# Performance work log

Hardware: AMD Instinct MI355X
Metric: run time of the kernel (lower is better)

## Reference

```python
import jax, jax.numpy as jnp
import numpy as np

N_NODES = 200000
N_PATCHES = 256
TIMESTEPS = 12
NHID = 16
HORIZON = 12
IN_DIM = NHID * TIMESTEPS + TIMESTEPS  # 204


def setup_inputs() -> dict:
    key = jax.random.key(0)
    ks = jax.random.split(key, 6)
    mixer_x = jax.random.normal(ks[0], (1, TIMESTEPS, N_PATCHES, NHID), dtype=jnp.float32)
    features = jax.random.normal(ks[1], (N_NODES, TIMESTEPS), dtype=jnp.float32)
    W1 = jax.random.normal(ks[2], (IN_DIM, IN_DIM), dtype=jnp.float32) * (1.0 / np.sqrt(IN_DIM))
    b1 = jnp.zeros((IN_DIM,), dtype=jnp.float32)
    W2 = jax.random.normal(ks[3], (IN_DIM, HORIZON), dtype=jnp.float32) * (1.0 / np.sqrt(IN_DIM))
    b2 = jnp.zeros((HORIZON,), dtype=jnp.float32)
    node_patch = jax.random.randint(ks[4], (N_NODES,), 0, N_PATCHES, dtype=jnp.int32)
    return {"mixer_x": mixer_x, "features": features, "W1": W1, "b1": b1,
            "W2": W2, "b2": b2, "node_patch": node_patch}


def reference(mixer_x, features, W1, b1, W2, b2, node_patch):
    # mixer_x: (b, t, p, f) -> per-patch flattened features 'b p (t f)'
    b, t, p, f = mixer_x.shape
    patch_feat = jnp.transpose(mixer_x, (0, 2, 1, 3)).reshape(b, p, t * f)
    # per-node gather of its patch's features: (b, N, t*f)
    g = jnp.take(patch_feat, node_patch, axis=1)
    # node features broadcast over batch: (b, N, t)
    node_x = jnp.broadcast_to(features[None], (b,) + features.shape)
    x = jnp.concatenate([g, node_x], axis=-1)  # (b, N, in_dim)
    h = jax.nn.relu(jnp.einsum('bni,ij->bnj', x, W1) + b1)
    out = jnp.einsum('bnh,ho->bno', h, W2) + b2  # (1, N, horizon)
    return out
```

## Files before the change

kernel.cpp:

```cpp
#include <hip/hip_runtime.h>
#include <hip/hip_bf16.h>

#define N_NODES   200000
#define N_PATCHES 256
#define TSTEPS    12
#define NHID      16
#define HORIZON   12
#define GDIM      192
#define IN_DIM    204
#define NCHUNKS   6250
#define K2_THREADS 512
#define TOTAL_WAVES 2048
#define TBL_U4    6528

typedef __attribute__((ext_vector_type(8)))  short        bf16x8;
typedef __attribute__((ext_vector_type(16))) float        f32x16;
typedef __attribute__((ext_vector_type(4)))  unsigned int u32x4;

__device__ __forceinline__ unsigned int pk2(float lo, float hi) {
    unsigned short l = __builtin_bit_cast(unsigned short, __float2bfloat16(lo));
    unsigned short h = __builtin_bit_cast(unsigned short, __float2bfloat16(hi));
    return ((unsigned int)h << 16) | (unsigned int)l;
}

__device__ __forceinline__ bf16x8 frag_of(unsigned int a, unsigned int b,
                                          unsigned int c, unsigned int d) {
    u32x4 u; u[0] = a; u[1] = b; u[2] = c; u[3] = d;
    return __builtin_bit_cast(bf16x8, u);
}

__device__ __forceinline__ float bf16bits_lo(unsigned int w) {
    return __builtin_bit_cast(float, w << 16);
}
__device__ __forceinline__ float bf16bits_hi(unsigned int w) {
    return __builtin_bit_cast(float, w & 0xffff0000u);
}

__device__ __forceinline__ void gload_lds16(const uint4* g, uint4* l) {
    __builtin_amdgcn_global_load_lds(
        (const __attribute__((address_space(1))) unsigned int*)g,
        (__attribute__((address_space(3))) unsigned int*)l,
        16, 0, 0);
}

__device__ __forceinline__ float ldW1f(const float* __restrict__ W1, int k, int j) {
    const bool ok = (k < TSTEPS) && (j < IN_DIM);
    const int  idx = ok ? ((GDIM + k) * IN_DIM + j) : 0;
    const float v = W1[idx];
    return ok ? v : 0.0f;
}
__device__ __forceinline__ float ldW2t(const float* __restrict__ W2, int j, int o) {
    const bool ok = (j < IN_DIM) && (o < HORIZON);
    const int  idx = ok ? (j * HORIZON + o) : 0;
    const float v = W2[idx];
    return ok ? v : 0.0f;
}

__global__ __launch_bounds__(1024) void precompute(
    const float* __restrict__ mixer_x,
    const float* __restrict__ W1,
    const float* __restrict__ b1,
    const float* __restrict__ W2,
    unsigned short* __restrict__ patch_hb,
    u32x4* __restrict__ wfrag)
{
    const int blk = blockIdx.x;
    const int tid = threadIdx.x;

    if (blk == N_PATCHES) {
        const int lane = tid & 63;
        const int g    = tid >> 6;
        const int jl   = lane & 31;
        const int kb   = 4 * (lane >> 5);
        for (int f = g; f < 20; f += 16) {
            u32x4 u;
            if (f < 7) {
                const int j = f * 32 + jl;
                u[0] = pk2(ldW1f(W1, kb + 0,  j), ldW1f(W1, kb + 1,  j));
                u[1] = pk2(ldW1f(W1, kb + 2,  j), ldW1f(W1, kb + 3,  j));
                u[2] = pk2(ldW1f(W1, kb + 8,  j), ldW1f(W1, kb + 9,  j));
                u[3] = pk2(ldW1f(W1, kb + 10, j), ldW1f(W1, kb + 11, j));
            } else {
                const int j0 = (f - 7) * 16 + kb;
                u[0] = pk2(ldW2t(W2, j0 + 0,  jl), ldW2t(W2, j0 + 1,  jl));
                u[1] = pk2(ldW2t(W2, j0 + 2,  jl), ldW2t(W2, j0 + 3,  jl));
                u[2] = pk2(ldW2t(W2, j0 + 8,  jl), ldW2t(W2, j0 + 9,  jl));
                u[3] = pk2(ldW2t(W2, j0 + 10, jl), ldW2t(W2, j0 + 11, jl));
            }
            wfrag[f * 64 + lane] = u;
        }
        return;
    }

    __shared__ float xs[GDIM];
    __shared__ float partial[3 * IN_DIM];
    const int p = blk;
    const int j = tid & 255;
    const int q = tid >> 8;

    if (tid < GDIM) {
        const int t = tid >> 4, f = tid & 15;
        xs[tid] = mixer_x[(t * N_PATCHES + p) * NHID + f];
    }
    __syncthreads();

    float acc = 0.0f;
    if (j < IN_DIM) {
        acc = (q == 0) ? b1[j] : 0.0f;
        const int ibase = q * 48;
#pragma unroll 16
        for (int i = 0; i < 48; ++i)
            acc = fmaf(xs[ibase + i], W1[(ibase + i) * IN_DIM + j], acc);
        if (q > 0) partial[(q - 1) * IN_DIM + j] = acc;
    }
    __syncthreads();
    if (q == 0 && j < IN_DIM) {
        const float v = acc + partial[j] + partial[IN_DIM + j] + partial[2 * IN_DIM + j];
        patch_hb[p * IN_DIM + j] =
            __builtin_bit_cast(unsigned short, __float2bfloat16(v));
    }
}

__global__ __launch_bounds__(512) void node_mlp_mfma(
    const float* __restrict__ features,
    const int*   __restrict__ node_patch,
    const unsigned short* __restrict__ patch_hb,
    const u32x4* __restrict__ wfrag,
    const float* __restrict__ b2,
    float* __restrict__ out)
{
    __shared__ unsigned short smem[N_PATCHES * IN_DIM];

    const int tid  = threadIdx.x;
    const int lane = tid & 63;
    const int wid  = tid >> 6;
    const int jl   = lane & 31;
    const int hi   = lane >> 5;

    int c = blockIdx.x * 8 + wid;
    float4 fa, fb, fc; int p;
    {
        const float4* fp = (const float4*)(features + (c * 32 + jl) * TSTEPS);
        fa = fp[0]; fb = fp[1]; fc = fp[2];
        p  = node_patch[c * 32 + jl];
    }

    bf16x8 A1f[7], A2f[13];
#pragma unroll
    for (int f = 0; f < 7; ++f)
        A1f[f] = __builtin_bit_cast(bf16x8, wfrag[f * 64 + lane]);
#pragma unroll
    for (int f = 0; f < 13; ++f)
        A2f[f] = __builtin_bit_cast(bf16x8, wfrag[(7 + f) * 64 + lane]);

    const float4 b2A = *(const float4*)(b2 + 4 * hi);
    const float4 b2B = *(const float4*)(b2 + 8);

    {
        const uint4* src = (const uint4*)patch_hb;
        uint4* dst = (uint4*)smem;
#pragma unroll
        for (int k = 0; k < 13; ++k) {
            const int i = tid + k * K2_THREADS;
            if (i < TBL_U4) gload_lds16(src + i, dst + i);
        }
    }
    __syncthreads();

    while (true) {
        const int  cn    = c + TOTAL_WAVES;
        const bool haveN = (cn < NCHUNKS);
        float4 fa2, fb2, fc2; int p2 = 0;
        if (haveN) {
            const float4* fq = (const float4*)(features + (cn * 32 + jl) * TSTEPS);
            fa2 = fq[0]; fb2 = fq[1]; fc2 = fq[2];
            p2  = node_patch[cn * 32 + jl];
        }

        const bf16x8 B1 = frag_of(hi ? pk2(fb.x, fb.y) : pk2(fa.x, fa.y),
                                  hi ? pk2(fb.z, fb.w) : pk2(fa.z, fa.w),
                                  hi ? 0u              : pk2(fc.x, fc.y),
                                  hi ? 0u              : pk2(fc.z, fc.w));

        const unsigned short* row = smem + p * IN_DIM;

        f32x16 oE, oO;
#pragma unroll
        for (int e = 0; e < 16; ++e) { oE[e] = 0.0f; oO[e] = 0.0f; }

#pragma unroll
        for (int t = 0; t < 7; ++t) {
            f32x16 acc;
#pragma unroll
            for (int G = 0; G < 4; ++G) {
                const int eoff = t * 32 + 8 * G + 4 * hi;
                const bool ok  = (eoff <= 200);
                const uint2 r  = *(const uint2*)(row + (ok ? eoff : 0));
                acc[4 * G + 0] = ok ? bf16bits_lo(r.x) : 0.0f;
                acc[4 * G + 1] = ok ? bf16bits_hi(r.x) : 0.0f;
                acc[4 * G + 2] = ok ? bf16bits_lo(r.y) : 0.0f;
                acc[4 * G + 3] = ok ? bf16bits_hi(r.y) : 0.0f;
            }

            acc = __builtin_amdgcn_mfma_f32_32x32x16_bf16(A1f[t], B1, acc, 0, 0, 0);

            const bf16x8 ba = frag_of(
                pk2(fmaxf(acc[0], 0.f), fmaxf(acc[1], 0.f)),
                pk2(fmaxf(acc[2], 0.f), fmaxf(acc[3], 0.f)),
                pk2(fmaxf(acc[4], 0.f), fmaxf(acc[5], 0.f)),
                pk2(fmaxf(acc[6], 0.f), fmaxf(acc[7], 0.f)));
            oE = __builtin_amdgcn_mfma_f32_32x32x16_bf16(A2f[2 * t], ba, oE, 0, 0, 0);

            if (t < 6) {
                const bf16x8 bb = frag_of(
                    pk2(fmaxf(acc[8],  0.f), fmaxf(acc[9],  0.f)),
                    pk2(fmaxf(acc[10], 0.f), fmaxf(acc[11], 0.f)),
                    pk2(fmaxf(acc[12], 0.f), fmaxf(acc[13], 0.f)),
                    pk2(fmaxf(acc[14], 0.f), fmaxf(acc[15], 0.f)));
                oO = __builtin_amdgcn_mfma_f32_32x32x16_bf16(A2f[2 * t + 1], bb, oO, 0, 0, 0);
            }
        }

        {
            const int node = c * 32 + jl;
            float* orow = out + node * HORIZON;
            const float s0 = oE[0] + oO[0], s1 = oE[1] + oO[1];
            const float s2 = oE[2] + oO[2], s3 = oE[3] + oO[3];
            if (hi == 0) {
                const float s4 = oE[4] + oO[4], s5 = oE[5] + oO[5];
                const float s6 = oE[6] + oO[6], s7 = oE[7] + oO[7];
                *(float4*)(orow + 0) = make_float4(s0 + b2A.x, s1 + b2A.y,
                                                   s2 + b2A.z, s3 + b2A.w);
                *(float4*)(orow + 8) = make_float4(s4 + b2B.x, s5 + b2B.y,
                                                   s6 + b2B.z, s7 + b2B.w);
            } else {
                *(float4*)(orow + 4) = make_float4(s0 + b2A.x, s1 + b2A.y,
                                                   s2 + b2A.z, s3 + b2A.w);
            }
        }

        if (!haveN) break;
        fa = fa2; fb = fb2; fc = fc2; p = p2; c = cn;
    }
}

extern "C" void kernel_launch(void* const* d_in, const int* in_sizes, int n_in,
                              void* d_out, int out_size, void* d_ws, size_t ws_size,
                              hipStream_t stream) {
    const float* mixer_x    = (const float*)d_in[0];
    const float* features   = (const float*)d_in[1];
    const float* W1         = (const float*)d_in[2];
    const float* b1         = (const float*)d_in[3];
    const float* W2         = (const float*)d_in[4];
    const float* b2         = (const float*)d_in[5];
    const int*   node_patch = (const int*)d_in[6];
    float* out = (float*)d_out;

    unsigned short* patch_hb = (unsigned short*)d_ws;
    u32x4*          wfrag    = (u32x4*)((char*)d_ws + 104448);

    precompute<<<257, 1024, 0, stream>>>(mixer_x, W1, b1, W2, patch_hb, wfrag);

    node_mlp_mfma<<<256, K2_THREADS, 0, stream>>>(features, node_patch,
                                                  patch_hb, wfrag, b2, out);
}
```

Before: 25.84 us.

## Use 768-thread blocks, hardware bf16 pack instruction, and single output accumulator

```diff
diff --git a/kernel.cpp b/kernel.cpp
--- a/kernel.cpp
+++ b/kernel.cpp
@@ -9,8 +9,8 @@
 #define GDIM      192
 #define IN_DIM    204
 #define NCHUNKS   6250
-#define K2_THREADS 512
-#define TOTAL_WAVES 2048
+#define K2_THREADS 768
+#define K2_WAVES_TOTAL 3072
 #define TBL_U4    6528
 
 typedef __attribute__((ext_vector_type(8)))  short        bf16x8;
@@ -21,6 +21,12 @@
     unsigned short l = __builtin_bit_cast(unsigned short, __float2bfloat16(lo));
     unsigned short h = __builtin_bit_cast(unsigned short, __float2bfloat16(hi));
     return ((unsigned int)h << 16) | (unsigned int)l;
+}
+
+__device__ __forceinline__ unsigned int cvtpk(float lo, float hi) {
+    unsigned int r;
+    asm("v_cvt_pk_bf16_f32 %0, %1, %2" : "=v"(r) : "v"(lo), "v"(hi));
+    return r;
 }
 
 __device__ __forceinline__ bf16x8 frag_of(unsigned int a, unsigned int b,
@@ -121,7 +127,7 @@
     }
 }
 
-__global__ __launch_bounds__(512) void node_mlp_mfma(
+__global__ __launch_bounds__(K2_THREADS) void node_mlp_mfma(
     const float* __restrict__ features,
     const int*   __restrict__ node_patch,
     const unsigned short* __restrict__ patch_hb,
@@ -137,7 +143,7 @@
     const int jl   = lane & 31;
     const int hi   = lane >> 5;
 
-    int c = blockIdx.x * 8 + wid;
+    int c = blockIdx.x * 12 + wid;
     float4 fa, fb, fc; int p;
     {
         const float4* fp = (const float4*)(features + (c * 32 + jl) * TSTEPS);
@@ -160,7 +166,7 @@
         const uint4* src = (const uint4*)patch_hb;
         uint4* dst = (uint4*)smem;
 #pragma unroll
-        for (int k = 0; k < 13; ++k) {
+        for (int k = 0; k < 9; ++k) {
             const int i = tid + k * K2_THREADS;
             if (i < TBL_U4) gload_lds16(src + i, dst + i);
         }
@@ -168,7 +174,7 @@
     __syncthreads();
 
     while (true) {
-        const int  cn    = c + TOTAL_WAVES;
+        const int  cn    = c + K2_WAVES_TOTAL;
         const bool haveN = (cn < NCHUNKS);
         float4 fa2, fb2, fc2; int p2 = 0;
         if (haveN) {
@@ -177,16 +183,16 @@
             p2  = node_patch[cn * 32 + jl];
         }
 
-        const bf16x8 B1 = frag_of(hi ? pk2(fb.x, fb.y) : pk2(fa.x, fa.y),
-                                  hi ? pk2(fb.z, fb.w) : pk2(fa.z, fa.w),
-                                  hi ? 0u              : pk2(fc.x, fc.y),
-                                  hi ? 0u              : pk2(fc.z, fc.w));
+        const bf16x8 B1 = frag_of(hi ? cvtpk(fb.x, fb.y) : cvtpk(fa.x, fa.y),
+                                  hi ? cvtpk(fb.z, fb.w) : cvtpk(fa.z, fa.w),
+                                  hi ? 0u                : cvtpk(fc.x, fc.y),
+                                  hi ? 0u                : cvtpk(fc.z, fc.w));
 
         const unsigned short* row = smem + p * IN_DIM;
 
-        f32x16 oE, oO;
-#pragma unroll
-        for (int e = 0; e < 16; ++e) { oE[e] = 0.0f; oO[e] = 0.0f; }
+        f32x16 oacc;
+#pragma unroll
+        for (int e = 0; e < 16; ++e) oacc[e] = 0.0f;
 
 #pragma unroll
         for (int t = 0; t < 7; ++t) {
@@ -205,37 +211,33 @@
             acc = __builtin_amdgcn_mfma_f32_32x32x16_bf16(A1f[t], B1, acc, 0, 0, 0);
 
             const bf16x8 ba = frag_of(
-                pk2(fmaxf(acc[0], 0.f), fmaxf(acc[1], 0.f)),
-                pk2(fmaxf(acc[2], 0.f), fmaxf(acc[3], 0.f)),
-                pk2(fmaxf(acc[4], 0.f), fmaxf(acc[5], 0.f)),
-                pk2(fmaxf(acc[6], 0.f), fmaxf(acc[7], 0.f)));
-            oE = __builtin_amdgcn_mfma_f32_32x32x16_bf16(A2f[2 * t], ba, oE, 0, 0, 0);
+                cvtpk(fmaxf(acc[0], 0.f), fmaxf(acc[1], 0.f)),
+                cvtpk(fmaxf(acc[2], 0.f), fmaxf(acc[3], 0.f)),
+                cvtpk(fmaxf(acc[4], 0.f), fmaxf(acc[5], 0.f)),
+                cvtpk(fmaxf(acc[6], 0.f), fmaxf(acc[7], 0.f)));
+            oacc = __builtin_amdgcn_mfma_f32_32x32x16_bf16(A2f[2 * t], ba, oacc, 0, 0, 0);
 
             if (t < 6) {
                 const bf16x8 bb = frag_of(
-                    pk2(fmaxf(acc[8],  0.f), fmaxf(acc[9],  0.f)),
-                    pk2(fmaxf(acc[10], 0.f), fmaxf(acc[11], 0.f)),
-                    pk2(fmaxf(acc[12], 0.f), fmaxf(acc[13], 0.f)),
-                    pk2(fmaxf(acc[14], 0.f), fmaxf(acc[15], 0.f)));
-                oO = __builtin_amdgcn_mfma_f32_32x32x16_bf16(A2f[2 * t + 1], bb, oO, 0, 0, 0);
+                    cvtpk(fmaxf(acc[8],  0.f), fmaxf(acc[9],  0.f)),
+                    cvtpk(fmaxf(acc[10], 0.f), fmaxf(acc[11], 0.f)),
+                    cvtpk(fmaxf(acc[12], 0.f), fmaxf(acc[13], 0.f)),
+                    cvtpk(fmaxf(acc[14], 0.f), fmaxf(acc[15], 0.f)));
+                oacc = __builtin_amdgcn_mfma_f32_32x32x16_bf16(A2f[2 * t + 1], bb, oacc, 0, 0, 0);
             }
         }
 
         {
             const int node = c * 32 + jl;
             float* orow = out + node * HORIZON;
-            const float s0 = oE[0] + oO[0], s1 = oE[1] + oO[1];
-            const float s2 = oE[2] + oO[2], s3 = oE[3] + oO[3];
             if (hi == 0) {
-                const float s4 = oE[4] + oO[4], s5 = oE[5] + oO[5];
-                const float s6 = oE[6] + oO[6], s7 = oE[7] + oO[7];
-                *(float4*)(orow + 0) = make_float4(s0 + b2A.x, s1 + b2A.y,
-                                                   s2 + b2A.z, s3 + b2A.w);
-                *(float4*)(orow + 8) = make_float4(s4 + b2B.x, s5 + b2B.y,
-                                                   s6 + b2B.z, s7 + b2B.w);
+                *(float4*)(orow + 0) = make_float4(oacc[0] + b2A.x, oacc[1] + b2A.y,
+                                                   oacc[2] + b2A.z, oacc[3] + b2A.w);
+                *(float4*)(orow + 8) = make_float4(oacc[4] + b2B.x, oacc[5] + b2B.y,
+                                                   oacc[6] + b2B.z, oacc[7] + b2B.w);
             } else {
-                *(float4*)(orow + 4) = make_float4(s0 + b2A.x, s1 + b2A.y,
-                                                   s2 + b2A.z, s3 + b2A.w);
+                *(float4*)(orow + 4) = make_float4(oacc[0] + b2A.x, oacc[1] + b2A.y,
+                                                   oacc[2] + b2A.z, oacc[3] + b2A.w);
             }
         }
 
```

Result: no change. 26.14 us (+1.1%).
